# Kernel optimization log

Measured on AMD Instinct MI355X. Metric: run time of the kernel, lower is better.

## Reference

```python
import jax, jax.numpy as jnp
import numpy as np

N = 50000
E = 800000
D_IN = 128
D_HID = 256


def setup_inputs() -> dict:
    key = jax.random.key(0)
    ks = jax.random.split(key, 12)
    s = 0.02
    return {
        "node_features": jax.random.normal(ks[0], (N, D_IN), dtype=jnp.float32),
        "edge_index": jax.random.randint(ks[1], (2, E), 0, N, dtype=jnp.int64),
        # layer 0 (input_dim -> hidden)
        "eps0": jnp.zeros((), dtype=jnp.float32),
        "W1_0": jax.random.normal(ks[2], (D_IN, D_HID), dtype=jnp.float32) * s,
        "b1_0": jnp.zeros((D_HID,), dtype=jnp.float32),
        "W2_0": jax.random.normal(ks[3], (D_HID, D_HID), dtype=jnp.float32) * s,
        "b2_0": jnp.zeros((D_HID,), dtype=jnp.float32),
        # layer 1 (hidden -> hidden)
        "eps1": jnp.zeros((), dtype=jnp.float32),
        "W1_1": jax.random.normal(ks[4], (D_HID, D_HID), dtype=jnp.float32) * s,
        "b1_1": jnp.zeros((D_HID,), dtype=jnp.float32),
        "W2_1": jax.random.normal(ks[5], (D_HID, D_HID), dtype=jnp.float32) * s,
        "b2_1": jnp.zeros((D_HID,), dtype=jnp.float32),
        # fc_out (hidden -> input_dim)
        "Wo": jax.random.normal(ks[6], (D_HID, D_IN), dtype=jnp.float32) * s,
        "bo": jnp.zeros((D_IN,), dtype=jnp.float32),
    }


def _gin_layer(x, src, dst, eps, W1, b1, W2, b2):
    # gather neighbor features + scatter-add into destination nodes
    agg = jnp.zeros_like(x).at[dst].add(x[src])  # [N, d]
    h = (1.0 + eps) * x + agg
    h = jax.nn.relu(h @ W1 + b1)
    return h @ W2 + b2


def reference(node_features, edge_index, eps0, W1_0, b1_0, W2_0, b2_0,
              eps1, W1_1, b1_1, W2_1, b2_1, Wo, bo):
    src, dst = edge_index[0], edge_index[1]
    h = _gin_layer(node_features, src, dst, eps0, W1_0, b1_0, W2_0, b2_0)
    h = _gin_layer(h, src, dst, eps1, W1_1, b1_1, W2_1, b2_1)
    return h @ Wo + bo  # [N, input_dim]
```

## Files before the change

kernel.cpp:

```cpp
#include <hip/hip_runtime.h>

#define NN 50000
#define NE 800000
#define DIN 128
#define DHID 256
#define MAXDEG 128

typedef __bf16 bf16x8 __attribute__((ext_vector_type(8)));
typedef float f32x4 __attribute__((ext_vector_type(4)));

static __device__ __forceinline__ unsigned short f2bf(float f) {
    unsigned u = __float_as_uint(f);
    unsigned r = 0x7fffu + ((u >> 16) & 1u);
    return (unsigned short)((u + r) >> 16);
}
static __device__ __forceinline__ float blo(unsigned u) { return __uint_as_float(u << 16); }
static __device__ __forceinline__ float bhi(unsigned u) { return __uint_as_float(u & 0xffff0000u); }


__global__ void bucket_kernel(const int* __restrict__ src, const int* __restrict__ dst,
                              int* __restrict__ cnt, int* __restrict__ srcs, int E) {
    int i8 = (blockIdx.x * blockDim.x + threadIdx.x) * 8;
    if (i8 >= E) return;
    int4 da = *(const int4*)&dst[i8];
    int4 db = *(const int4*)&dst[i8 + 4];
    int4 sa = *(const int4*)&src[i8];
    int4 sb = *(const int4*)&src[i8 + 4];
    int t0 = atomicAdd(&cnt[da.x], 1);
    int t1 = atomicAdd(&cnt[da.y], 1);
    int t2 = atomicAdd(&cnt[da.z], 1);
    int t3 = atomicAdd(&cnt[da.w], 1);
    int t4 = atomicAdd(&cnt[db.x], 1);
    int t5 = atomicAdd(&cnt[db.y], 1);
    int t6 = atomicAdd(&cnt[db.z], 1);
    int t7 = atomicAdd(&cnt[db.w], 1);
    if (t0 < MAXDEG) srcs[(size_t)da.x * MAXDEG + t0] = sa.x;
    if (t1 < MAXDEG) srcs[(size_t)da.y * MAXDEG + t1] = sa.y;
    if (t2 < MAXDEG) srcs[(size_t)da.z * MAXDEG + t2] = sa.z;
    if (t3 < MAXDEG) srcs[(size_t)da.w * MAXDEG + t3] = sa.w;
    if (t4 < MAXDEG) srcs[(size_t)db.x * MAXDEG + t4] = sb.x;
    if (t5 < MAXDEG) srcs[(size_t)db.y * MAXDEG + t5] = sb.y;
    if (t6 < MAXDEG) srcs[(size_t)db.z * MAXDEG + t6] = sb.z;
    if (t7 < MAXDEG) srcs[(size_t)db.w * MAXDEG + t7] = sb.w;
}


__global__ void prep_kernel(const float* __restrict__ x, unsigned short* __restrict__ xb,
                            int* __restrict__ cnt,
                            const float* __restrict__ W1_0, const float* __restrict__ W2_0,
                            const float* __restrict__ W1_1, const float* __restrict__ W2_1,
                            const float* __restrict__ Wo,
                            unsigned short* __restrict__ w10t, unsigned short* __restrict__ w20t,
                            unsigned short* __restrict__ w11t, unsigned short* __restrict__ w21t,
                            unsigned short* __restrict__ wot) {
    int i = blockIdx.x * blockDim.x + threadIdx.x;
    if (i < NN) cnt[i] = 0;
    if (i < 262144) {
        const float* W; unsigned short* Wt; int K, N, idx;
        if (i < 32768)        { W = W1_0; Wt = w10t; K = 128; N = 256; idx = i; }
        else if (i < 98304)   { W = W2_0; Wt = w20t; K = 256; N = 256; idx = i - 32768; }
        else if (i < 163840)  { W = W1_1; Wt = w11t; K = 256; N = 256; idx = i - 98304; }
        else if (i < 229376)  { W = W2_1; Wt = w21t; K = 256; N = 256; idx = i - 163840; }
        else                  { W = Wo;   Wt = wot;  K = 256; N = 128; idx = i - 229376; }
        int k = idx / N;
        int n = idx - k * N;
        Wt[(size_t)n * K + k] = f2bf(W[idx]);
    }
    if (i * 4 < NN * DIN) {
        float4 v = *(const float4*)(x + (size_t)i * 4);
        ushort4 o;
        o.x = f2bf(v.x); o.y = f2bf(v.y); o.z = f2bf(v.z); o.w = f2bf(v.w);
        *(ushort4*)(xb + (size_t)i * 4) = o;
    }
}


template <int D>
__global__ void agg_bf16_kernel(const unsigned short* __restrict__ x, const int* __restrict__ cnt,
                                const int* __restrict__ srcs, const float* __restrict__ eps_p,
                                unsigned short* __restrict__ out, int n) {
    constexpr int G = (D == 128) ? 4 : 2;
    constexpr int L = 64 / G;
    constexpr int RQ = D / 8;
    int tid = blockIdx.x * blockDim.x + threadIdx.x;
    int wid = tid >> 6;
    int lane = threadIdx.x & 63;
    int group = lane / L;
    int li = lane % L;
    int node = wid * G + group;
    if (node >= n) return;
    int deg = cnt[node]; if (deg > MAXDEG) deg = MAXDEG;
    const int* sp = srcs + (size_t)node * MAXDEG;
    const uint4* xp = (const uint4*)x;
    float e = 1.0f + eps_p[0];

    float a[8], b[8];
    #pragma unroll
    for (int j = 0; j < 8; j++) { a[j] = 0.f; b[j] = 0.f; }

    int i = 0;
    for (; i + 4 <= deg; i += 4) {
        int4 s = *(const int4*)&sp[i];
        uint4 v0 = xp[(size_t)s.x * RQ + li];
        uint4 v1 = xp[(size_t)s.y * RQ + li];
        uint4 v2 = xp[(size_t)s.z * RQ + li];
        uint4 v3 = xp[(size_t)s.w * RQ + li];
        a[0] += blo(v0.x); a[1] += bhi(v0.x); a[2] += blo(v0.y); a[3] += bhi(v0.y);
        a[4] += blo(v0.z); a[5] += bhi(v0.z); a[6] += blo(v0.w); a[7] += bhi(v0.w);
        b[0] += blo(v1.x); b[1] += bhi(v1.x); b[2] += blo(v1.y); b[3] += bhi(v1.y);
        b[4] += blo(v1.z); b[5] += bhi(v1.z); b[6] += blo(v1.w); b[7] += bhi(v1.w);
        a[0] += blo(v2.x); a[1] += bhi(v2.x); a[2] += blo(v2.y); a[3] += bhi(v2.y);
        a[4] += blo(v2.z); a[5] += bhi(v2.z); a[6] += blo(v2.w); a[7] += bhi(v2.w);
        b[0] += blo(v3.x); b[1] += bhi(v3.x); b[2] += blo(v3.y); b[3] += bhi(v3.y);
        b[4] += blo(v3.z); b[5] += bhi(v3.z); b[6] += blo(v3.w); b[7] += bhi(v3.w);
    }
    for (; i < deg; i++) {
        uint4 v = xp[(size_t)sp[i] * RQ + li];
        a[0] += blo(v.x); a[1] += bhi(v.x); a[2] += blo(v.y); a[3] += bhi(v.y);
        a[4] += blo(v.z); a[5] += bhi(v.z); a[6] += blo(v.w); a[7] += bhi(v.w);
    }
    uint4 xv = xp[(size_t)node * RQ + li];
    a[0] += b[0] + e * blo(xv.x); a[1] += b[1] + e * bhi(xv.x);
    a[2] += b[2] + e * blo(xv.y); a[3] += b[3] + e * bhi(xv.y);
    a[4] += b[4] + e * blo(xv.z); a[5] += b[5] + e * bhi(xv.z);
    a[6] += b[6] + e * blo(xv.w); a[7] += b[7] + e * bhi(xv.w);
    uint4 o;
    o.x = (unsigned)f2bf(a[0]) | ((unsigned)f2bf(a[1]) << 16);
    o.y = (unsigned)f2bf(a[2]) | ((unsigned)f2bf(a[3]) << 16);
    o.z = (unsigned)f2bf(a[4]) | ((unsigned)f2bf(a[5]) << 16);
    o.w = (unsigned)f2bf(a[6]) | ((unsigned)f2bf(a[7]) << 16);
    ((uint4*)out)[(size_t)node * RQ + li] = o;
}


template <int K1, int THREE>
__global__ __launch_bounds__(256) void mlp_fused(
        const unsigned short* __restrict__ A,
        const unsigned short* __restrict__ W1t, const float* __restrict__ b1,
        const unsigned short* __restrict__ W2t, const float* __restrict__ b2,
        const unsigned short* __restrict__ W3t, const float* __restrict__ b3,
        unsigned short* __restrict__ Cb, float* __restrict__ Cf, int M) {
    constexpr int NKS1 = K1 / 32;
    __shared__ __align__(16) unsigned short H[64 * 256];

    const int lane = threadIdx.x & 63;
    const int w = threadIdx.x >> 6;
    const int quad = lane >> 4;
    const int l16 = lane & 15;
    const size_t rowbase = (size_t)blockIdx.x * 64;

    f32x4 acc[4][4];

    #pragma unroll
    for (int j = 0; j < 4; j++)
        #pragma unroll
        for (int nt = 0; nt < 4; nt++) acc[j][nt] = (f32x4)(0.f);
    #pragma unroll 2
    for (int ks = 0; ks < NKS1; ks++) {
        bf16x8 bw[4];
        #pragma unroll
        for (int nt = 0; nt < 4; nt++)
            bw[nt] = *(const bf16x8*)&W1t[(size_t)(w * 64 + nt * 16 + l16) * K1 + ks * 32 + quad * 8];
        #pragma unroll
        for (int j = 0; j < 4; j++) {
            bf16x8 af = *(const bf16x8*)&A[(rowbase + j * 16 + l16) * K1 + ks * 32 + quad * 8];
            #pragma unroll
            for (int nt = 0; nt < 4; nt++)
                acc[j][nt] = __builtin_amdgcn_mfma_f32_16x16x32_bf16(bw[nt], af, acc[j][nt], 0, 0, 0);
        }
    }
    {
        f32x4 bvv[4];
        #pragma unroll
        for (int nt = 0; nt < 4; nt++)
            bvv[nt] = *(const f32x4*)&b1[w * 64 + nt * 16 + quad * 4];
        #pragma unroll
        for (int j = 0; j < 4; j++) {
            int r = j * 16 + l16;
            #pragma unroll
            for (int nt = 0; nt < 4; nt++) {
                f32x4 v = acc[j][nt] + bvv[nt];
                v[0] = fmaxf(v[0], 0.f); v[1] = fmaxf(v[1], 0.f);
                v[2] = fmaxf(v[2], 0.f); v[3] = fmaxf(v[3], 0.f);
                int c = w * 8 + nt * 2 + (quad >> 1);
                int cs = c ^ (r & 7);
                uint2 o;
                o.x = (unsigned)f2bf(v[0]) | ((unsigned)f2bf(v[1]) << 16);
                o.y = (unsigned)f2bf(v[2]) | ((unsigned)f2bf(v[3]) << 16);
                *(uint2*)&H[r * 256 + cs * 8 + (quad & 1) * 4] = o;
            }
        }
    }
    __syncthreads();

    #pragma unroll
    for (int j = 0; j < 4; j++)
        #pragma unroll
        for (int nt = 0; nt < 4; nt++) acc[j][nt] = (f32x4)(0.f);
    #pragma unroll 2
    for (int ks = 0; ks < 8; ks++) {
        bf16x8 bw[4];
        #pragma unroll
        for (int nt = 0; nt < 4; nt++)
            bw[nt] = *(const bf16x8*)&W2t[(size_t)(w * 64 + nt * 16 + l16) * 256 + ks * 32 + quad * 8];
        #pragma unroll
        for (int j = 0; j < 4; j++) {
            int r = j * 16 + l16;
            int cs = (ks * 4 + quad) ^ (r & 7);
            bf16x8 af = *(const bf16x8*)&H[r * 256 + cs * 8];
            #pragma unroll
            for (int nt = 0; nt < 4; nt++)
                acc[j][nt] = __builtin_amdgcn_mfma_f32_16x16x32_bf16(bw[nt], af, acc[j][nt], 0, 0, 0);
        }
    }
    {
        f32x4 bvv[4];
        #pragma unroll
        for (int nt = 0; nt < 4; nt++)
            bvv[nt] = *(const f32x4*)&b2[w * 64 + nt * 16 + quad * 4];
        if constexpr (!THREE) {
            #pragma unroll
            for (int j = 0; j < 4; j++) {
                size_t gm = rowbase + j * 16 + l16;
                if (gm < (size_t)M) {
                    #pragma unroll
                    for (int nt = 0; nt < 4; nt++) {
                        f32x4 v = acc[j][nt] + bvv[nt];
                        uint2 o;
                        o.x = (unsigned)f2bf(v[0]) | ((unsigned)f2bf(v[1]) << 16);
                        o.y = (unsigned)f2bf(v[2]) | ((unsigned)f2bf(v[3]) << 16);
                        *(uint2*)&Cb[gm * 256 + w * 64 + nt * 16 + quad * 4] = o;
                    }
                }
            }
        } else {
            __syncthreads();
            #pragma unroll
            for (int j = 0; j < 4; j++) {
                int r = j * 16 + l16;
                #pragma unroll
                for (int nt = 0; nt < 4; nt++) {
                    f32x4 v = acc[j][nt] + bvv[nt];
                    int c = w * 8 + nt * 2 + (quad >> 1);
                    int cs = c ^ (r & 7);
                    uint2 o;
                    o.x = (unsigned)f2bf(v[0]) | ((unsigned)f2bf(v[1]) << 16);
                    o.y = (unsigned)f2bf(v[2]) | ((unsigned)f2bf(v[3]) << 16);
                    *(uint2*)&H[r * 256 + cs * 8 + (quad & 1) * 4] = o;
                }
            }
            __syncthreads();
        }
    }

    if constexpr (THREE) {
        f32x4 acc3[4][2];
        #pragma unroll
        for (int j = 0; j < 4; j++)
            #pragma unroll
            for (int nt = 0; nt < 2; nt++) acc3[j][nt] = (f32x4)(0.f);
        #pragma unroll 2
        for (int ks = 0; ks < 8; ks++) {
            bf16x8 bw[2];
            #pragma unroll
            for (int nt = 0; nt < 2; nt++)
                bw[nt] = *(const bf16x8*)&W3t[(size_t)(w * 32 + nt * 16 + l16) * 256 + ks * 32 + quad * 8];
            #pragma unroll
            for (int j = 0; j < 4; j++) {
                int r = j * 16 + l16;
                int cs = (ks * 4 + quad) ^ (r & 7);
                bf16x8 af = *(const bf16x8*)&H[r * 256 + cs * 8];
                #pragma unroll
                for (int nt = 0; nt < 2; nt++)
                    acc3[j][nt] = __builtin_amdgcn_mfma_f32_16x16x32_bf16(bw[nt], af, acc3[j][nt], 0, 0, 0);
            }
        }
        f32x4 bv3[2];
        #pragma unroll
        for (int nt = 0; nt < 2; nt++)
            bv3[nt] = *(const f32x4*)&b3[w * 32 + nt * 16 + quad * 4];
        #pragma unroll
        for (int j = 0; j < 4; j++) {
            size_t gm = rowbase + j * 16 + l16;
            if (gm < (size_t)M) {
                #pragma unroll
                for (int nt = 0; nt < 2; nt++) {
                    f32x4 v = acc3[j][nt] + bv3[nt];
                    *(f32x4*)&Cf[gm * 128 + w * 32 + nt * 16 + quad * 4] = v;
                }
            }
        }
    }
}


static inline size_t align256(size_t v) { return (v + 255) & ~(size_t)255; }

extern "C" void kernel_launch(void* const* d_in, const int* in_sizes, int n_in,
                              void* d_out, int out_size, void* d_ws, size_t ws_size,
                              hipStream_t stream) {
    const float* x        = (const float*)d_in[0];
    const int*   ei       = (const int*)d_in[1];
    const float* eps0     = (const float*)d_in[2];
    const float* W1_0     = (const float*)d_in[3];
    const float* b1_0     = (const float*)d_in[4];
    const float* W2_0     = (const float*)d_in[5];
    const float* b2_0     = (const float*)d_in[6];
    const float* eps1     = (const float*)d_in[7];
    const float* W1_1     = (const float*)d_in[8];
    const float* b1_1     = (const float*)d_in[9];
    const float* W2_1     = (const float*)d_in[10];
    const float* b2_1     = (const float*)d_in[11];
    const float* Wo       = (const float*)d_in[12];
    const float* bo       = (const float*)d_in[13];
    float* out            = (float*)d_out;

    const int* srcE = ei;
    const int* dstE = ei + NE;

    char* p = (char*)d_ws;
    size_t o = 0;
    int* cnt  = (int*)(p + o); o = align256(o + (size_t)NN * 4);
    int* srcs = (int*)(p + o); o = align256(o + (size_t)NN * MAXDEG * 4);
    unsigned short* xb   = (unsigned short*)(p + o); o = align256(o + (size_t)NN * DIN * 2);
    unsigned short* w10t = (unsigned short*)(p + o); o = align256(o + (size_t)DHID * DIN * 2);
    unsigned short* w20t = (unsigned short*)(p + o); o = align256(o + (size_t)DHID * DHID * 2);
    unsigned short* w11t = (unsigned short*)(p + o); o = align256(o + (size_t)DHID * DHID * 2);
    unsigned short* w21t = (unsigned short*)(p + o); o = align256(o + (size_t)DHID * DHID * 2);
    unsigned short* wot  = (unsigned short*)(p + o); o = align256(o + (size_t)DIN * DHID * 2);
    unsigned short* bufA = (unsigned short*)(p + o); o = align256(o + (size_t)NN * DHID * 2 + 65536);
    unsigned short* bufB = (unsigned short*)(p + o); o = align256(o + (size_t)NN * DHID * 2 + 65536);

    prep_kernel<<<(NN * DIN / 4 + 255) / 256, 256, 0, stream>>>(
        x, xb, cnt, W1_0, W2_0, W1_1, W2_1, Wo, w10t, w20t, w11t, w21t, wot);
    bucket_kernel<<<(NE / 8 + 255) / 256, 256, 0, stream>>>(srcE, dstE, cnt, srcs, NE);

    int aggBlocks128 = ((NN + 3) / 4 + 3) / 4;
    int aggBlocks256 = ((NN + 1) / 2 + 3) / 4;
    int mlpBlocks = (NN + 63) / 64;

    agg_bf16_kernel<DIN><<<aggBlocks128, 256, 0, stream>>>(xb, cnt, srcs, eps0, bufA, NN);
    mlp_fused<128, 0><<<mlpBlocks, 256, 0, stream>>>(
        bufA, w10t, b1_0, w20t, b2_0, nullptr, nullptr, bufB, nullptr, NN);

    agg_bf16_kernel<DHID><<<aggBlocks256, 256, 0, stream>>>(bufB, cnt, srcs, eps1, bufA, NN);
    mlp_fused<256, 1><<<mlpBlocks, 256, 0, stream>>>(
        bufA, w11t, b1_1, w21t, b2_1, wot, bo, nullptr, out, NN);
}
```

Measured before the change: 331.1 us.

## Fuse neighbor aggregation into the per-layer MLP kernels via shared memory

Each GIN layer's gather-sum aggregation now runs inside the MLP kernel, writing the aggregated 64-row tile straight into swizzled LDS instead of round-tripping it through a global bf16 buffer. This removes two kernel launches and the global write/read of the aggregated activations. The aggregation inner loop is also unrolled to 8 neighbors to put more loads in flight. In exchange, LDS per block grows (up to 64KB in layer 1), which can cut occupancy and leaves the latency-bound gather with fewer concurrent waves to hide memory stalls.

```diff
diff --git a/kernel.cpp b/kernel.cpp
--- a/kernel.cpp
+++ b/kernel.cpp
@@ -75,36 +75,27 @@
 }
 
 
-template <int D>
-__global__ void agg_bf16_kernel(const unsigned short* __restrict__ x, const int* __restrict__ cnt,
-                                const int* __restrict__ srcs, const float* __restrict__ eps_p,
-                                unsigned short* __restrict__ out, int n) {
-    constexpr int G = (D == 128) ? 4 : 2;
-    constexpr int L = 64 / G;
-    constexpr int RQ = D / 8;
-    int tid = blockIdx.x * blockDim.x + threadIdx.x;
-    int wid = tid >> 6;
-    int lane = threadIdx.x & 63;
-    int group = lane / L;
-    int li = lane % L;
-    int node = wid * G + group;
-    if (node >= n) return;
+template <int RQ>
+static __device__ __forceinline__ uint4 gather_node(
+        const uint4* __restrict__ xp, const int* __restrict__ cnt,
+        const int* __restrict__ srcs, float e, int node, int li) {
+    float a[8], b[8];
+    #pragma unroll
+    for (int j = 0; j < 8; j++) { a[j] = 0.f; b[j] = 0.f; }
     int deg = cnt[node]; if (deg > MAXDEG) deg = MAXDEG;
     const int* sp = srcs + (size_t)node * MAXDEG;
-    const uint4* xp = (const uint4*)x;
-    float e = 1.0f + eps_p[0];
-
-    float a[8], b[8];
-    #pragma unroll
-    for (int j = 0; j < 8; j++) { a[j] = 0.f; b[j] = 0.f; }
-
     int i = 0;
-    for (; i + 4 <= deg; i += 4) {
-        int4 s = *(const int4*)&sp[i];
-        uint4 v0 = xp[(size_t)s.x * RQ + li];
-        uint4 v1 = xp[(size_t)s.y * RQ + li];
-        uint4 v2 = xp[(size_t)s.z * RQ + li];
-        uint4 v3 = xp[(size_t)s.w * RQ + li];
+    for (; i + 8 <= deg; i += 8) {
+        int4 s0 = *(const int4*)&sp[i];
+        int4 s1 = *(const int4*)&sp[i + 4];
+        uint4 v0 = xp[(size_t)s0.x * RQ + li];
+        uint4 v1 = xp[(size_t)s0.y * RQ + li];
+        uint4 v2 = xp[(size_t)s0.z * RQ + li];
+        uint4 v3 = xp[(size_t)s0.w * RQ + li];
+        uint4 v4 = xp[(size_t)s1.x * RQ + li];
+        uint4 v5 = xp[(size_t)s1.y * RQ + li];
+        uint4 v6 = xp[(size_t)s1.z * RQ + li];
+        uint4 v7 = xp[(size_t)s1.w * RQ + li];
         a[0] += blo(v0.x); a[1] += bhi(v0.x); a[2] += blo(v0.y); a[3] += bhi(v0.y);
         a[4] += blo(v0.z); a[5] += bhi(v0.z); a[6] += blo(v0.w); a[7] += bhi(v0.w);
         b[0] += blo(v1.x); b[1] += bhi(v1.x); b[2] += blo(v1.y); b[3] += bhi(v1.y);
@@ -113,6 +104,14 @@
         a[4] += blo(v2.z); a[5] += bhi(v2.z); a[6] += blo(v2.w); a[7] += bhi(v2.w);
         b[0] += blo(v3.x); b[1] += bhi(v3.x); b[2] += blo(v3.y); b[3] += bhi(v3.y);
         b[4] += blo(v3.z); b[5] += bhi(v3.z); b[6] += blo(v3.w); b[7] += bhi(v3.w);
+        a[0] += blo(v4.x); a[1] += bhi(v4.x); a[2] += blo(v4.y); a[3] += bhi(v4.y);
+        a[4] += blo(v4.z); a[5] += bhi(v4.z); a[6] += blo(v4.w); a[7] += bhi(v4.w);
+        b[0] += blo(v5.x); b[1] += bhi(v5.x); b[2] += blo(v5.y); b[3] += bhi(v5.y);
+        b[4] += blo(v5.z); b[5] += bhi(v5.z); b[6] += blo(v5.w); b[7] += bhi(v5.w);
+        a[0] += blo(v6.x); a[1] += bhi(v6.x); a[2] += blo(v6.y); a[3] += bhi(v6.y);
+        a[4] += blo(v6.z); a[5] += bhi(v6.z); a[6] += blo(v6.w); a[7] += bhi(v6.w);
+        b[0] += blo(v7.x); b[1] += bhi(v7.x); b[2] += blo(v7.y); b[3] += bhi(v7.y);
+        b[4] += blo(v7.z); b[5] += bhi(v7.z); b[6] += blo(v7.w); b[7] += bhi(v7.w);
     }
     for (; i < deg; i++) {
         uint4 v = xp[(size_t)sp[i] * RQ + li];
@@ -129,25 +128,42 @@
     o.y = (unsigned)f2bf(a[2]) | ((unsigned)f2bf(a[3]) << 16);
     o.z = (unsigned)f2bf(a[4]) | ((unsigned)f2bf(a[5]) << 16);
     o.w = (unsigned)f2bf(a[6]) | ((unsigned)f2bf(a[7]) << 16);
-    ((uint4*)out)[(size_t)node * RQ + li] = o;
-}
-
-
-template <int K1, int THREE>
-__global__ __launch_bounds__(256) void mlp_fused(
-        const unsigned short* __restrict__ A,
+    return o;
+}
+
+
+__global__ __launch_bounds__(256) void fused_layer0(
+        const unsigned short* __restrict__ xb, const int* __restrict__ cnt,
+        const int* __restrict__ srcs, const float* __restrict__ eps_p,
         const unsigned short* __restrict__ W1t, const float* __restrict__ b1,
         const unsigned short* __restrict__ W2t, const float* __restrict__ b2,
-        const unsigned short* __restrict__ W3t, const float* __restrict__ b3,
-        unsigned short* __restrict__ Cb, float* __restrict__ Cf, int M) {
-    constexpr int NKS1 = K1 / 32;
-    __shared__ __align__(16) unsigned short H[64 * 256];
-
-    const int lane = threadIdx.x & 63;
-    const int w = threadIdx.x >> 6;
+        unsigned short* __restrict__ Cb, int M) {
+    __shared__ __align__(16) unsigned short H0[64 * 128];
+    __shared__ __align__(16) unsigned short H1[64 * 256];
+
+    const int tid = threadIdx.x;
+    const int lane = tid & 63;
+    const int w = tid >> 6;
     const int quad = lane >> 4;
     const int l16 = lane & 15;
     const size_t rowbase = (size_t)blockIdx.x * 64;
+    const float e = 1.0f + eps_p[0];
+
+    {
+        const int group = tid >> 4;
+        const int li = tid & 15;
+        const uint4* xp = (const uint4*)xb;
+        #pragma unroll
+        for (int iter = 0; iter < 4; iter++) {
+            int r = iter * 16 + group;
+            int node = (int)rowbase + r;
+            uint4 o = make_uint4(0, 0, 0, 0);
+            if (node < M) o = gather_node<16>(xp, cnt, srcs, e, node, li);
+            int cs = li ^ (r & 7);
+            *(uint4*)&H0[r * 128 + cs * 8] = o;
+        }
+    }
+    __syncthreads();
 
     f32x4 acc[4][4];
 
@@ -156,14 +172,16 @@
         #pragma unroll
         for (int nt = 0; nt < 4; nt++) acc[j][nt] = (f32x4)(0.f);
     #pragma unroll 2
-    for (int ks = 0; ks < NKS1; ks++) {
+    for (int ks = 0; ks < 4; ks++) {
         bf16x8 bw[4];
         #pragma unroll
         for (int nt = 0; nt < 4; nt++)
-            bw[nt] = *(const bf16x8*)&W1t[(size_t)(w * 64 + nt * 16 + l16) * K1 + ks * 32 + quad * 8];
-        #pragma unroll
-        for (int j = 0; j < 4; j++) {
-            bf16x8 af = *(const bf16x8*)&A[(rowbase + j * 16 + l16) * K1 + ks * 32 + quad * 8];
+            bw[nt] = *(const bf16x8*)&W1t[(size_t)(w * 64 + nt * 16 + l16) * 128 + ks * 32 + quad * 8];
+        #pragma unroll
+        for (int j = 0; j < 4; j++) {
+            int r = j * 16 + l16;
+            int cs = (ks * 4 + quad) ^ (r & 7);
+            bf16x8 af = *(const bf16x8*)&H0[r * 128 + cs * 8];
             #pragma unroll
             for (int nt = 0; nt < 4; nt++)
                 acc[j][nt] = __builtin_amdgcn_mfma_f32_16x16x32_bf16(bw[nt], af, acc[j][nt], 0, 0, 0);
@@ -187,7 +205,7 @@
                 uint2 o;
                 o.x = (unsigned)f2bf(v[0]) | ((unsigned)f2bf(v[1]) << 16);
                 o.y = (unsigned)f2bf(v[2]) | ((unsigned)f2bf(v[3]) << 16);
-                *(uint2*)&H[r * 256 + cs * 8 + (quad & 1) * 4] = o;
+                *(uint2*)&H1[r * 256 + cs * 8 + (quad & 1) * 4] = o;
             }
         }
     }
@@ -207,7 +225,7 @@
         for (int j = 0; j < 4; j++) {
             int r = j * 16 + l16;
             int cs = (ks * 4 + quad) ^ (r & 7);
-            bf16x8 af = *(const bf16x8*)&H[r * 256 + cs * 8];
+            bf16x8 af = *(const bf16x8*)&H1[r * 256 + cs * 8];
             #pragma unroll
             for (int nt = 0; nt < 4; nt++)
                 acc[j][nt] = __builtin_amdgcn_mfma_f32_16x16x32_bf16(bw[nt], af, acc[j][nt], 0, 0, 0);
@@ -218,76 +236,179 @@
         #pragma unroll
         for (int nt = 0; nt < 4; nt++)
             bvv[nt] = *(const f32x4*)&b2[w * 64 + nt * 16 + quad * 4];
-        if constexpr (!THREE) {
-            #pragma unroll
-            for (int j = 0; j < 4; j++) {
-                size_t gm = rowbase + j * 16 + l16;
-                if (gm < (size_t)M) {
-                    #pragma unroll
-                    for (int nt = 0; nt < 4; nt++) {
-                        f32x4 v = acc[j][nt] + bvv[nt];
-                        uint2 o;
-                        o.x = (unsigned)f2bf(v[0]) | ((unsigned)f2bf(v[1]) << 16);
-                        o.y = (unsigned)f2bf(v[2]) | ((unsigned)f2bf(v[3]) << 16);
-                        *(uint2*)&Cb[gm * 256 + w * 64 + nt * 16 + quad * 4] = o;
-                    }
-                }
-            }
-        } else {
-            __syncthreads();
-            #pragma unroll
-            for (int j = 0; j < 4; j++) {
-                int r = j * 16 + l16;
+        #pragma unroll
+        for (int j = 0; j < 4; j++) {
+            size_t gm = rowbase + j * 16 + l16;
+            if (gm < (size_t)M) {
                 #pragma unroll
                 for (int nt = 0; nt < 4; nt++) {
                     f32x4 v = acc[j][nt] + bvv[nt];
-                    int c = w * 8 + nt * 2 + (quad >> 1);
-                    int cs = c ^ (r & 7);
                     uint2 o;
                     o.x = (unsigned)f2bf(v[0]) | ((unsigned)f2bf(v[1]) << 16);
                     o.y = (unsigned)f2bf(v[2]) | ((unsigned)f2bf(v[3]) << 16);
-                    *(uint2*)&H[r * 256 + cs * 8 + (quad & 1) * 4] = o;
+                    *(uint2*)&Cb[gm * 256 + w * 64 + nt * 16 + quad * 4] = o;
                 }
             }
-            __syncthreads();
-        }
-    }
-
-    if constexpr (THREE) {
-        f32x4 acc3[4][2];
-        #pragma unroll
-        for (int j = 0; j < 4; j++)
-            #pragma unroll
-            for (int nt = 0; nt < 2; nt++) acc3[j][nt] = (f32x4)(0.f);
-        #pragma unroll 2
-        for (int ks = 0; ks < 8; ks++) {
-            bf16x8 bw[2];
+        }
+    }
+}
+
+
+__global__ __launch_bounds__(256) void fused_layer1(
+        const unsigned short* __restrict__ hb, const int* __restrict__ cnt,
+        const int* __restrict__ srcs, const float* __restrict__ eps_p,
+        const unsigned short* __restrict__ W1t, const float* __restrict__ b1,
+        const unsigned short* __restrict__ W2t, const float* __restrict__ b2,
+        const unsigned short* __restrict__ W3t, const float* __restrict__ b3,
+        float* __restrict__ Cf, int M) {
+    __shared__ __align__(16) unsigned short H0[64 * 256];
+    __shared__ __align__(16) unsigned short H1[64 * 256];
+
+    const int tid = threadIdx.x;
+    const int lane = tid & 63;
+    const int w = tid >> 6;
+    const int quad = lane >> 4;
+    const int l16 = lane & 15;
+    const size_t rowbase = (size_t)blockIdx.x * 64;
+    const float e = 1.0f + eps_p[0];
+
+    {
+        const int group = tid >> 5;
+        const int li = tid & 31;
+        const uint4* xp = (const uint4*)hb;
+        #pragma unroll
+        for (int iter = 0; iter < 8; iter++) {
+            int r = iter * 8 + group;
+            int node = (int)rowbase + r;
+            uint4 o = make_uint4(0, 0, 0, 0);
+            if (node < M) o = gather_node<32>(xp, cnt, srcs, e, node, li);
+            int cs = li ^ (r & 7);
+            *(uint4*)&H0[r * 256 + cs * 8] = o;
+        }
+    }
+    __syncthreads();
+
+    f32x4 acc[4][4];
+
+    #pragma unroll
+    for (int j = 0; j < 4; j++)
+        #pragma unroll
+        for (int nt = 0; nt < 4; nt++) acc[j][nt] = (f32x4)(0.f);
+    #pragma unroll 2
+    for (int ks = 0; ks < 8; ks++) {
+        bf16x8 bw[4];
+        #pragma unroll
+        for (int nt = 0; nt < 4; nt++)
+            bw[nt] = *(const bf16x8*)&W1t[(size_t)(w * 64 + nt * 16 + l16) * 256 + ks * 32 + quad * 8];
+        #pragma unroll
+        for (int j = 0; j < 4; j++) {
+            int r = j * 16 + l16;
+            int cs = (ks * 4 + quad) ^ (r & 7);
+            bf16x8 af = *(const bf16x8*)&H0[r * 256 + cs * 8];
+            #pragma unroll
+            for (int nt = 0; nt < 4; nt++)
+                acc[j][nt] = __builtin_amdgcn_mfma_f32_16x16x32_bf16(bw[nt], af, acc[j][nt], 0, 0, 0);
+        }
+    }
+    {
+        f32x4 bvv[4];
+        #pragma unroll
+        for (int nt = 0; nt < 4; nt++)
+            bvv[nt] = *(const f32x4*)&b1[w * 64 + nt * 16 + quad * 4];
+        #pragma unroll
+        for (int j = 0; j < 4; j++) {
+            int r = j * 16 + l16;
+            #pragma unroll
+            for (int nt = 0; nt < 4; nt++) {
+                f32x4 v = acc[j][nt] + bvv[nt];
+                v[0] = fmaxf(v[0], 0.f); v[1] = fmaxf(v[1], 0.f);
+                v[2] = fmaxf(v[2], 0.f); v[3] = fmaxf(v[3], 0.f);
+                int c = w * 8 + nt * 2 + (quad >> 1);
+                int cs = c ^ (r & 7);
+                uint2 o;
+                o.x = (unsigned)f2bf(v[0]) | ((unsigned)f2bf(v[1]) << 16);
+                o.y = (unsigned)f2bf(v[2]) | ((unsigned)f2bf(v[3]) << 16);
+                *(uint2*)&H1[r * 256 + cs * 8 + (quad & 1) * 4] = o;
+            }
+        }
+    }
+    __syncthreads();
+
+    #pragma unroll
+    for (int j = 0; j < 4; j++)
+        #pragma unroll
+        for (int nt = 0; nt < 4; nt++) acc[j][nt] = (f32x4)(0.f);
+    #pragma unroll 2
+    for (int ks = 0; ks < 8; ks++) {
+        bf16x8 bw[4];
+        #pragma unroll
+        for (int nt = 0; nt < 4; nt++)
+            bw[nt] = *(const bf16x8*)&W2t[(size_t)(w * 64 + nt * 16 + l16) * 256 + ks * 32 + quad * 8];
+        #pragma unroll
+        for (int j = 0; j < 4; j++) {
+            int r = j * 16 + l16;
+            int cs = (ks * 4 + quad) ^ (r & 7);
+            bf16x8 af = *(const bf16x8*)&H1[r * 256 + cs * 8];
+            #pragma unroll
+            for (int nt = 0; nt < 4; nt++)
+                acc[j][nt] = __builtin_amdgcn_mfma_f32_16x16x32_bf16(bw[nt], af, acc[j][nt], 0, 0, 0);
+        }
+    }
+    {
+        f32x4 bvv[4];
+        #pragma unroll
+        for (int nt = 0; nt < 4; nt++)
+            bvv[nt] = *(const f32x4*)&b2[w * 64 + nt * 16 + quad * 4];
+        #pragma unroll
+        for (int j = 0; j < 4; j++) {
+            int r = j * 16 + l16;
+            #pragma unroll
+            for (int nt = 0; nt < 4; nt++) {
+                f32x4 v = acc[j][nt] + bvv[nt];
+                int c = w * 8 + nt * 2 + (quad >> 1);
+                int cs = c ^ (r & 7);
+                uint2 o;
+                o.x = (unsigned)f2bf(v[0]) | ((unsigned)f2bf(v[1]) << 16);
+                o.y = (unsigned)f2bf(v[2]) | ((unsigned)f2bf(v[3]) << 16);
+                *(uint2*)&H0[r * 256 + cs * 8 + (quad & 1) * 4] = o;
+            }
+        }
+    }
+    __syncthreads();
+
+    f32x4 acc3[4][2];
+    #pragma unroll
+    for (int j = 0; j < 4; j++)
+        #pragma unroll
+        for (int nt = 0; nt < 2; nt++) acc3[j][nt] = (f32x4)(0.f);
+    #pragma unroll 2
+    for (int ks = 0; ks < 8; ks++) {
+        bf16x8 bw[2];
+        #pragma unroll
+        for (int nt = 0; nt < 2; nt++)
+            bw[nt] = *(const bf16x8*)&W3t[(size_t)(w * 32 + nt * 16 + l16) * 256 + ks * 32 + quad * 8];
+        #pragma unroll
+        for (int j = 0; j < 4; j++) {
+            int r = j * 16 + l16;
+            int cs = (ks * 4 + quad) ^ (r & 7);
+            bf16x8 af = *(const bf16x8*)&H0[r * 256 + cs * 8];
             #pragma unroll
             for (int nt = 0; nt < 2; nt++)
-                bw[nt] = *(const bf16x8*)&W3t[(size_t)(w * 32 + nt * 16 + l16) * 256 + ks * 32 + quad * 8];
-            #pragma unroll
-            for (int j = 0; j < 4; j++) {
-                int r = j * 16 + l16;
-                int cs = (ks * 4 + quad) ^ (r & 7);
-                bf16x8 af = *(const bf16x8*)&H[r * 256 + cs * 8];
-                #pragma unroll
-                for (int nt = 0; nt < 2; nt++)
-                    acc3[j][nt] = __builtin_amdgcn_mfma_f32_16x16x32_bf16(bw[nt], af, acc3[j][nt], 0, 0, 0);
-            }
-        }
-        f32x4 bv3[2];
-        #pragma unroll
-        for (int nt = 0; nt < 2; nt++)
-            bv3[nt] = *(const f32x4*)&b3[w * 32 + nt * 16 + quad * 4];
-        #pragma unroll
-        for (int j = 0; j < 4; j++) {
-            size_t gm = rowbase + j * 16 + l16;
-            if (gm < (size_t)M) {
-                #pragma unroll
-                for (int nt = 0; nt < 2; nt++) {
-                    f32x4 v = acc3[j][nt] + bv3[nt];
-                    *(f32x4*)&Cf[gm * 128 + w * 32 + nt * 16 + quad * 4] = v;
-                }
+                acc3[j][nt] = __builtin_amdgcn_mfma_f32_16x16x32_bf16(bw[nt], af, acc3[j][nt], 0, 0, 0);
+        }
+    }
+    f32x4 bv3[2];
+    #pragma unroll
+    for (int nt = 0; nt < 2; nt++)
+        bv3[nt] = *(const f32x4*)&b3[w * 32 + nt * 16 + quad * 4];
+    #pragma unroll
+    for (int j = 0; j < 4; j++) {
+        size_t gm = rowbase + j * 16 + l16;
+        if (gm < (size_t)M) {
+            #pragma unroll
+            for (int nt = 0; nt < 2; nt++) {
+                f32x4 v = acc3[j][nt] + bv3[nt];
+                *(f32x4*)&Cf[gm * 128 + w * 32 + nt * 16 + quad * 4] = v;
             }
         }
     }
@@ -328,22 +449,17 @@
     unsigned short* w11t = (unsigned short*)(p + o); o = align256(o + (size_t)DHID * DHID * 2);
     unsigned short* w21t = (unsigned short*)(p + o); o = align256(o + (size_t)DHID * DHID * 2);
     unsigned short* wot  = (unsigned short*)(p + o); o = align256(o + (size_t)DIN * DHID * 2);
-    unsigned short* bufA = (unsigned short*)(p + o); o = align256(o + (size_t)NN * DHID * 2 + 65536);
-    unsigned short* bufB = (unsigned short*)(p + o); o = align256(o + (size_t)NN * DHID * 2 + 65536);
+    unsigned short* bufB = (unsigned short*)(p + o); o = align256(o + (size_t)NN * DHID * 2);
 
     prep_kernel<<<(NN * DIN / 4 + 255) / 256, 256, 0, stream>>>(
         x, xb, cnt, W1_0, W2_0, W1_1, W2_1, Wo, w10t, w20t, w11t, w21t, wot);
     bucket_kernel<<<(NE / 8 + 255) / 256, 256, 0, stream>>>(srcE, dstE, cnt, srcs, NE);
 
-    int aggBlocks128 = ((NN + 3) / 4 + 3) / 4;
-    int aggBlocks256 = ((NN + 1) / 2 + 3) / 4;
-    int mlpBlocks = (NN + 63) / 64;
-
-    agg_bf16_kernel<DIN><<<aggBlocks128, 256, 0, stream>>>(xb, cnt, srcs, eps0, bufA, NN);
-    mlp_fused<128, 0><<<mlpBlocks, 256, 0, stream>>>(
-        bufA, w10t, b1_0, w20t, b2_0, nullptr, nullptr, bufB, nullptr, NN);
-
-    agg_bf16_kernel<DHID><<<aggBlocks256, 256, 0, stream>>>(bufB, cnt, srcs, eps1, bufA, NN);
-    mlp_fused<256, 1><<<mlpBlocks, 256, 0, stream>>>(
-        bufA, w11t, b1_1, w21t, b2_1, wot, bo, nullptr, out, NN);
-}
+    int blocks = (NN + 63) / 64;
+
+    fused_layer0<<<blocks, 256, 0, stream>>>(
+        xb, cnt, srcs, eps0, w10t, b1_0, w20t, b2_0, bufB, NN);
+
+    fused_layer1<<<blocks, 256, 0, stream>>>(
+        bufB, cnt, srcs, eps1, w11t, b1_1, w21t, b2_1, wot, bo, out, NN);
+}
```

Result: slower. 362.0 us (+9.3%).
